# Kernel tuning notes

Measured on AMD Instinct MI355X. Metric: run time of the kernel, lower is better.

## Reference

```python
import math
import jax, jax.numpy as jnp
import numpy as np

B, L, D = 8, 512, 32
SEQ_LEN = 512.0
N_PATCHES, N_REF = 16, 32
LAT, HM = 128, 4
FH, NL, FF = 8, 3, 128
PRED = 96

def _time_embed(t, d):
    # interleaved sin/cos embedding, matching PositionalEmbedding's div_term
    div = jnp.exp(jnp.arange(0, d, 2, dtype=jnp.float32) * (-math.log(10000.0) / d))
    ang = t[..., None] * div
    out = jnp.zeros(t.shape + (d,), dtype=jnp.float32)
    return out.at[..., 0::2].set(jnp.sin(ang)).at[..., 1::2].set(jnp.cos(ang))

def _layernorm(x, g, b):
    mu = jnp.mean(x, axis=-1, keepdims=True)
    var = jnp.var(x, axis=-1, keepdims=True)
    return (x - mu) / jnp.sqrt(var + 1e-5) * g + b

def _mha(z, Wq, Wk, Wv, Wo, bq, bk, bv, bo):
    N, S, dm = z.shape
    hd = dm // FH
    q = (z @ Wq + bq).reshape(N, S, FH, hd)
    k = (z @ Wk + bk).reshape(N, S, FH, hd)
    v = (z @ Wv + bv).reshape(N, S, FH, hd)
    s = jnp.einsum('nqhe,nkhe->nhqk', q, k) / math.sqrt(hd)
    a = jax.nn.softmax(s, axis=-1)
    o = jnp.einsum('nhqk,nkhe->nqhe', a, v).reshape(N, S, dm)
    return o @ Wo + bo

def _forward(x, x_mark, x_mask, Wq, Wk, W_out, b_out, f_Wq, f_Wk, f_Wv, f_Wo, f_bq, f_bk, f_bv, f_bo, f_ln1_g, f_ln1_b, f_W1, f_b1, f_W2, f_b2, f_ln2_g, f_ln2_b, ln_f_g, ln_f_b, W_lin, b_lin):
    t = x_mark[:, :, 0]                                   # [B, L] irregular timestamps in [0, SEQ_LEN]
    edges = jnp.linspace(0.0, SEQ_LEN, N_PATCHES + 1)
    refs = jnp.linspace(0.0, SEQ_LEN, N_REF * N_PATCHES).reshape(N_PATCHES, N_REF)
    obs_valid = jnp.sum(x_mask, axis=-1) > 0              # [B, L]
    dk = LAT // HM
    Kmat = (_time_embed(t, LAT) @ Wk).reshape(B, L, HM, dk)
    v = x * x_mask                                        # mask values like `v = v * m` in original
    reprs = []
    for i in range(N_PATCHES):  # fixed small structural loop
        # _split_patch equivalent: per-channel masked attention is permutation
        # invariant, so the sort/scatter compaction reduces to masking.
        in_patch = (t >= edges[i]) & (t <= edges[i + 1]) & obs_valid   # [B, L]
        Qi = (_time_embed(refs[i], LAT) @ Wq).reshape(N_REF, HM, dk)
        scores = jnp.einsum('rhe,blhe->bhrl', Qi, Kmat) / math.sqrt(dk)
        cmask = x_mask * in_patch[..., None].astype(x.dtype)           # [B, L, D]
        neg = jnp.where(cmask[:, None, None, :, :] > 0, 0.0, -1e9)     # [B,1,1,L,D]
        p = jax.nn.softmax(scores[..., None] + neg, axis=3)            # [B,H,R,L,D]
        attn = jnp.einsum('bhrld,bld->brhd', p, v)                     # [B,R,H,D]
        reprs.append(attn.reshape(B, N_REF, HM * D) @ W_out + b_out)   # [B,R,D]
    rp = jnp.stack(reprs, axis=1)                          # [B, NP, R, D]
    z = rp.transpose(0, 3, 1, 2).reshape(B * D, N_PATCHES, N_REF)
    z = z + _time_embed(jnp.arange(N_PATCHES, dtype=jnp.float32), N_REF)[None]
    for l in range(NL):
        a = _mha(z, f_Wq[l], f_Wk[l], f_Wv[l], f_Wo[l], f_bq[l], f_bk[l], f_bv[l], f_bo[l])
        z = _layernorm(z + a, f_ln1_g[l], f_ln1_b[l])
        y = jax.nn.gelu(z @ f_W1[l] + f_b1[l]) @ f_W2[l] + f_b2[l]
        z = _layernorm(z + y, f_ln2_g[l], f_ln2_b[l])
    z = _layernorm(z, ln_f_g, ln_f_b)
    emb = z.reshape(B, D, N_PATCHES, N_REF).transpose(0, 1, 3, 2)      # [B, D, R, NP]
    out = emb.reshape(B, D, N_REF * N_PATCHES) @ W_lin + b_lin         # [B, D, PRED]
    return out.transpose(0, 2, 1)                          # [B, PRED, D]

def setup_inputs():
    key = jax.random.key(0)
    ks = jax.random.split(key, 30)
    def w(i, shape, fan_in):
        return jax.random.normal(ks[i], shape, jnp.float32) / math.sqrt(fan_in)
    return {
        'x': jax.random.normal(ks[0], (B, L, D), jnp.float32),
        'x_mark': jnp.sort(jax.random.uniform(ks[1], (B, L, 1), jnp.float32) * SEQ_LEN, axis=1),
        'x_mask': (jax.random.uniform(ks[2], (B, L, D), jnp.float32) < 0.8).astype(jnp.float32),
        'Wq': w(3, (LAT, LAT), LAT),
        'Wk': w(4, (LAT, LAT), LAT),
        'W_out': w(5, (HM * D, D), HM * D),
        'b_out': jnp.zeros((D,), jnp.float32),
        'f_Wq': w(6, (NL, N_REF, N_REF), N_REF),
        'f_Wk': w(7, (NL, N_REF, N_REF), N_REF),
        'f_Wv': w(8, (NL, N_REF, N_REF), N_REF),
        'f_Wo': w(9, (NL, N_REF, N_REF), N_REF),
        'f_bq': jnp.zeros((NL, N_REF), jnp.float32),
        'f_bk': jnp.zeros((NL, N_REF), jnp.float32),
        'f_bv': jnp.zeros((NL, N_REF), jnp.float32),
        'f_bo': jnp.zeros((NL, N_REF), jnp.float32),
        'f_ln1_g': jnp.ones((NL, N_REF), jnp.float32),
        'f_ln1_b': jnp.zeros((NL, N_REF), jnp.float32),
        'f_W1': w(10, (NL, N_REF, FF), N_REF),
        'f_b1': jnp.zeros((NL, FF), jnp.float32),
        'f_W2': w(11, (NL, FF, N_REF), FF),
        'f_b2': jnp.zeros((NL, N_REF), jnp.float32),
        'f_ln2_g': jnp.ones((NL, N_REF), jnp.float32),
        'f_ln2_b': jnp.zeros((NL, N_REF), jnp.float32),
        'ln_f_g': jnp.ones((N_REF,), jnp.float32),
        'ln_f_b': jnp.zeros((N_REF,), jnp.float32),
        'W_lin': w(12, (N_REF * N_PATCHES, PRED), N_REF * N_PATCHES),
        'b_lin': jnp.zeros((PRED,), jnp.float32),
    }

def reference(x, x_mark, x_mask, Wq, Wk, W_out, b_out, f_Wq, f_Wk, f_Wv, f_Wo, f_bq, f_bk, f_bv, f_bo, f_ln1_g, f_ln1_b, f_W1, f_b1, f_W2, f_b2, f_ln2_g, f_ln2_b, ln_f_g, ln_f_b, W_lin, b_lin):
    return _forward(x, x_mark, x_mask, Wq, Wk, W_out, b_out, f_Wq, f_Wk, f_Wv, f_Wo, f_bq, f_bk, f_bv, f_bo, f_ln1_g, f_ln1_b, f_W1, f_b1, f_W2, f_b2, f_ln2_g, f_ln2_b, ln_f_g, ln_f_b, W_lin, b_lin)
```

## Files before the change

### kernel.cpp

```cpp
#include <hip/hip_runtime.h>
#include <math.h>


#define ISQ32 0.17677669529663687f
#define C128  (-0.07195578415606394f)
#define C32   (-0.28782313662425575f)

__launch_bounds__(256)
__global__ void k_embed_mm(const float* __restrict__ x_mark,
                           const float* __restrict__ Wk,
                           const float* __restrict__ Wq,
                           const float* __restrict__ x_mask,
                           float* __restrict__ Kmat,
                           float* __restrict__ Qall,
                           unsigned* __restrict__ obsBits) {
    if (blockIdx.x >= 144) {
        const int gt = (blockIdx.x - 144) * 256 + threadIdx.x;
        const int w = gt >> 6, lane = gt & 63;
        const int bl = w * 2 + (lane >> 5);
        const int d = lane & 31;
        const unsigned long long mm = __ballot(x_mask[bl * 32 + d] > 0.0f);
        if (lane == 0)  obsBits[w * 2]     = (unsigned)(mm & 0xffffffffull);
        if (lane == 32) obsBits[w * 2 + 1] = (unsigned)(mm >> 32);
        return;
    }
    __shared__ float sTe[32][128];
    const int wv = threadIdx.x >> 6;
    const int lane = threadIdx.x & 63;
    const int bb = blockIdx.x;
    const int row0 = bb * 32 + wv * 8;
    const float dv = __expf((float)(2 * lane) * C128);
    #pragma unroll
    for (int rr = 0; rr < 8; ++rr) {
        const int row = row0 + rr;
        const float t = (row < 4096) ? x_mark[row] : (float)(row - 4096) * (512.0f / 511.0f);
        const float ang = t * dv;
        sTe[wv * 8 + rr][2 * lane]     = __sinf(ang);
        sTe[wv * 8 + rr][2 * lane + 1] = __cosf(ang);
    }
    __syncthreads();
    const float* W = (bb < 128) ? Wk : Wq;
    float a0[8], a1[8];
    #pragma unroll
    for (int rr = 0; rr < 8; ++rr) { a0[rr] = 0.f; a1[rr] = 0.f; }
    for (int k = 0; k < 128; ++k) {
        const float wa = W[k * 128 + lane];
        const float wb = W[k * 128 + lane + 64];
        #pragma unroll
        for (int rr = 0; rr < 8; ++rr) {
            const float te = sTe[wv * 8 + rr][k];
            a0[rr] = fmaf(te, wa, a0[rr]);
            a1[rr] = fmaf(te, wb, a1[rr]);
        }
    }
    #pragma unroll
    for (int rr = 0; rr < 8; ++rr) {
        const int row = row0 + rr;
        float* outp = (row < 4096) ? (Kmat + row * 128) : (Qall + (row - 4096) * 128);
        outp[lane] = a0[rr];
        outp[lane + 64] = a1[rr];
    }
}

__launch_bounds__(256)
__global__ void k_patch_attn(const float* __restrict__ x,
                             const float* __restrict__ x_mark,
                             const unsigned* __restrict__ obsBits,
                             const float* __restrict__ Kmat,
                             const float* __restrict__ Qall,
                             float* __restrict__ attn) {
    __shared__ float sQ[32][36];
    __shared__ float sK[96][36];
    __shared__ float sX[96][36];
    __shared__ float sS[32][100];
    __shared__ unsigned sBits[96];
    __shared__ int sLo, sHi;
    __shared__ unsigned sAV;
    const int tid = threadIdx.x;
    const int h = blockIdx.x & 3;
    const int b = (blockIdx.x >> 2) & 7;
    const int i = blockIdx.x >> 5;
    const float e0 = 32.0f * (float)i, e1 = 32.0f * (float)(i + 1);
    if (tid == 0) { sLo = 512; sHi = -1; sAV = 0u; }
    __syncthreads();
    #pragma unroll
    for (int k = 0; k < 4; ++k) {
        const int idx = tid + 256 * k;
        sQ[idx >> 5][idx & 31] = Qall[(i * 32 + (idx >> 5)) * 128 + h * 32 + (idx & 31)];
    }
    {
        int mylo = 512, myhi = -1;
        unsigned mybits = 0u;
        #pragma unroll
        for (int k = 0; k < 2; ++k) {
            const int l = tid + 256 * k;
            const float t = x_mark[b * 512 + l];
            if (t >= e0 && t <= e1) {
                mylo = min(mylo, l);
                myhi = max(myhi, l);
                mybits |= obsBits[b * 512 + l];
            }
        }
        #pragma unroll
        for (int off = 32; off > 0; off >>= 1) {
            mylo = min(mylo, __shfl_xor(mylo, off));
            myhi = max(myhi, __shfl_xor(myhi, off));
            mybits |= __shfl_xor(mybits, off);
        }
        if ((tid & 63) == 0) {
            atomicMin(&sLo, mylo);
            atomicMax(&sHi, myhi);
            atomicOr(&sAV, mybits);
        }
    }
    __syncthreads();
    const int lo = sLo, hi = sHi;
    const int NA = hi - lo + 1;
    const unsigned av = sAV;
    const int r = tid >> 3, dg = tid & 7;

    if (NA >= 1 && NA <= 96 && av == 0xffffffffu) {
        if (tid < NA) sBits[tid] = obsBits[b * 512 + lo + tid];
        for (int idx = tid; idx < NA * 32; idx += 256) {
            const int ll = idx >> 5, c = idx & 31;
            sK[ll][c] = Kmat[(b * 512 + lo + ll) * 128 + h * 32 + c];
            sX[ll][c] = x[(b * 512 + lo + ll) * 32 + c];
        }
        __syncthreads();
        float m = -1e30f;
        for (int ll = dg; ll < NA; ll += 8) {
            float p0 = 0.f, p1 = 0.f, p2 = 0.f, p3 = 0.f;
            #pragma unroll
            for (int e = 0; e < 32; e += 4) {
                p0 = fmaf(sQ[r][e],     sK[ll][e],     p0);
                p1 = fmaf(sQ[r][e + 1], sK[ll][e + 1], p1);
                p2 = fmaf(sQ[r][e + 2], sK[ll][e + 2], p2);
                p3 = fmaf(sQ[r][e + 3], sK[ll][e + 3], p3);
            }
            const float s = (p0 + p1 + p2 + p3) * ISQ32;
            sS[r][ll] = s;
            m = fmaxf(m, s);
        }
        #pragma unroll
        for (int off = 4; off > 0; off >>= 1) m = fmaxf(m, __shfl_xor(m, off));
        for (int ll = dg; ll < NA; ll += 8) sS[r][ll] = __expf(sS[r][ll] - m);
        __syncthreads();
        float num0 = 0.f, num1 = 0.f, num2 = 0.f, num3 = 0.f;
        float den0 = 0.f, den1 = 0.f, den2 = 0.f, den3 = 0.f;
        for (int ll = 0; ll < NA; ++ll) {
            const float e = sS[r][ll];
            const unsigned bits = sBits[ll];
            if ((bits >> dg) & 1u)        { den0 += e; num0 = fmaf(e, sX[ll][dg],      num0); }
            if ((bits >> (dg + 8)) & 1u)  { den1 += e; num1 = fmaf(e, sX[ll][dg + 8],  num1); }
            if ((bits >> (dg + 16)) & 1u) { den2 += e; num2 = fmaf(e, sX[ll][dg + 16], num2); }
            if ((bits >> (dg + 24)) & 1u) { den3 += e; num3 = fmaf(e, sX[ll][dg + 24], num3); }
        }
        float* ap = attn + ((i * 8 + b) * 32 + r) * 128 + h * 32;
        ap[dg]      = num0 / den0;
        ap[dg + 8]  = num1 / den1;
        ap[dg + 16] = num2 / den2;
        ap[dg + 24] = num3 / den3;
    } else {
        float m = -1e30f;
        float num[4] = {0.f, 0.f, 0.f, 0.f}, den[4] = {0.f, 0.f, 0.f, 0.f};
        for (int l = 0; l < 512; ++l) {
            const float t = x_mark[b * 512 + l];
            const unsigned bits = obsBits[b * 512 + l];
            const bool inr = (t >= e0 && t <= e1);
            const unsigned effD = (inr ? bits : 0u) | ~av;
            if (effD == 0u) continue;
            const unsigned effN = effD & bits;
            const float* Kp = Kmat + (b * 512 + l) * 128 + h * 32;
            float a = 0.f;
            #pragma unroll
            for (int e2 = 0; e2 < 32; ++e2) a = fmaf(sQ[r][e2], Kp[e2], a);
            const float s = a * ISQ32;
            float eNew;
            if (s > m) {
                const float scale = __expf(m - s);
                #pragma unroll
                for (int jj = 0; jj < 4; ++jj) { den[jj] *= scale; num[jj] *= scale; }
                m = s;
                eNew = 1.0f;
            } else {
                eNew = __expf(s - m);
            }
            const float* xp = x + (b * 512 + l) * 32;
            #pragma unroll
            for (int jj = 0; jj < 4; ++jj) {
                const int d = dg + 8 * jj;
                if ((effD >> d) & 1u) den[jj] += eNew;
                if ((effN >> d) & 1u) num[jj] = fmaf(eNew, xp[d], num[jj]);
            }
        }
        float* ap = attn + ((i * 8 + b) * 32 + r) * 128 + h * 32;
        #pragma unroll
        for (int jj = 0; jj < 4; ++jj) ap[dg + 8 * jj] = num[jj] / den[jj];
    }
}

__global__ void k_reprs(const float* __restrict__ attn,
                        const float* __restrict__ W_out,
                        const float* __restrict__ b_out,
                        float* __restrict__ z) {
    __shared__ float sA[32][129];
    const int tid = threadIdx.x;
    const int b = blockIdx.x & 7;
    const int i = blockIdx.x >> 3;
    #pragma unroll
    for (int k = 0; k < 16; ++k) {
        const int idx = tid + 256 * k;
        sA[idx >> 7][idx & 127] = attn[(i * 8 + b) * 4096 + idx];
    }
    __syncthreads();
    const int r = tid & 31, dgrp = tid >> 5;
    float acc0 = 0.f, acc1 = 0.f, acc2 = 0.f, acc3 = 0.f;
    #pragma unroll 8
    for (int k = 0; k < 128; ++k) {
        const float a = sA[r][k];
        acc0 = fmaf(a, W_out[k * 32 + dgrp],      acc0);
        acc1 = fmaf(a, W_out[k * 32 + dgrp + 8],  acc1);
        acc2 = fmaf(a, W_out[k * 32 + dgrp + 16], acc2);
        acc3 = fmaf(a, W_out[k * 32 + dgrp + 24], acc3);
    }
    const float dv = expf((float)(2 * (r >> 1)) * C32);
    const float ang = (float)i * dv;
    const float pe = (r & 1) ? cosf(ang) : sinf(ang);
    const int base = i * 32 + r;
    z[(b * 32 + dgrp)      * 512 + base] = acc0 + b_out[dgrp]      + pe;
    z[(b * 32 + dgrp + 8)  * 512 + base] = acc1 + b_out[dgrp + 8]  + pe;
    z[(b * 32 + dgrp + 16) * 512 + base] = acc2 + b_out[dgrp + 16] + pe;
    z[(b * 32 + dgrp + 24) * 512 + base] = acc3 + b_out[dgrp + 24] + pe;
}

__launch_bounds__(1024, 1)
__global__ void k_former(const float* __restrict__ z,
                         const float* __restrict__ f_Wq, const float* __restrict__ f_Wk,
                         const float* __restrict__ f_Wv, const float* __restrict__ f_Wo,
                         const float* __restrict__ f_bq, const float* __restrict__ f_bk,
                         const float* __restrict__ f_bv, const float* __restrict__ f_bo,
                         const float* __restrict__ f_ln1_g, const float* __restrict__ f_ln1_b,
                         const float* __restrict__ f_W1, const float* __restrict__ f_b1,
                         const float* __restrict__ f_W2, const float* __restrict__ f_b2,
                         const float* __restrict__ f_ln2_g, const float* __restrict__ f_ln2_b,
                         const float* __restrict__ ln_f_g, const float* __restrict__ ln_f_b,
                         const float* __restrict__ W_lin, const float* __restrict__ b_lin,
                         float* __restrict__ out) {
    __shared__ float sZ[16][36];
    __shared__ float sKm[16][36], sVm[16][36], sOm[16][36];
    __shared__ float sH[16][132];
    __shared__ float sZf[512];
    __shared__ float sPart[8][96];
    const int tid = threadIdx.x;
    const int n = blockIdx.x;
    const int s = tid >> 6;
    const int lane = tid & 63;
    const int j = lane & 31;
    const int kh = lane >> 5;

    float zres = z[n * 512 + s * 32 + j];
    if (kh == 0) sZ[s][j] = zres;

    for (int l = 0; l < 3; ++l) {
        float q_reg;
        {
            float zr[16];
            #pragma unroll
            for (int k4 = 0; k4 < 4; ++k4) {
                const float4 zv = *(const float4*)&sZ[s][kh * 16 + 4 * k4];
                zr[4 * k4] = zv.x; zr[4 * k4 + 1] = zv.y; zr[4 * k4 + 2] = zv.z; zr[4 * k4 + 3] = zv.w;
            }
            #pragma unroll
            for (int m = 0; m < 3; ++m) {
                const float* Wm = ((m == 0) ? f_Wq : (m == 1) ? f_Wk : f_Wv) + l * 1024;
                float w[16];
                #pragma unroll
                for (int k = 0; k < 16; ++k) w[k] = Wm[(kh * 16 + k) * 32 + j];
                float acc = 0.f;
                #pragma unroll
                for (int k = 0; k < 16; ++k) acc = fmaf(zr[k], w[k], acc);
                acc += __shfl_xor(acc, 32);
                acc += ((m == 0) ? f_bq : (m == 1) ? f_bk : f_bv)[l * 32 + j];
                if (m == 0) q_reg = acc;
                else if (m == 1) { if (kh == 0) sKm[s][j] = acc; }
                else             { if (kh == 0) sVm[s][j] = acc; }
            }
        }
        __syncthreads();
        {
            const int hh = lane >> 3;
            const int kp = lane & 7;
            const int h4 = hh * 4;
            const float qx = __shfl(q_reg, h4);
            const float qy = __shfl(q_reg, h4 + 1);
            const float qz = __shfl(q_reg, h4 + 2);
            const float qw = __shfl(q_reg, h4 + 3);
            const float4 kv0 = *(const float4*)&sKm[2 * kp][h4];
            const float4 kv1 = *(const float4*)&sKm[2 * kp + 1][h4];
            float s0 = (qx * kv0.x + qy * kv0.y + qz * kv0.z + qw * kv0.w) * 0.5f;
            float s1 = (qx * kv1.x + qy * kv1.y + qz * kv1.z + qw * kv1.w) * 0.5f;
            float mx = fmaxf(s0, s1);
            #pragma unroll
            for (int off = 4; off > 0; off >>= 1) mx = fmaxf(mx, __shfl_xor(mx, off));
            const float e0 = __expf(s0 - mx), e1 = __expf(s1 - mx);
            float sum = e0 + e1;
            #pragma unroll
            for (int off = 4; off > 0; off >>= 1) sum += __shfl_xor(sum, off);
            const float4 vv0 = *(const float4*)&sVm[2 * kp][h4];
            const float4 vv1 = *(const float4*)&sVm[2 * kp + 1][h4];
            float o0 = e0 * vv0.x + e1 * vv1.x;
            float o1 = e0 * vv0.y + e1 * vv1.y;
            float o2 = e0 * vv0.z + e1 * vv1.z;
            float o3 = e0 * vv0.w + e1 * vv1.w;
            #pragma unroll
            for (int off = 4; off > 0; off >>= 1) {
                o0 += __shfl_xor(o0, off); o1 += __shfl_xor(o1, off);
                o2 += __shfl_xor(o2, off); o3 += __shfl_xor(o3, off);
            }
            if (kp == 0) {
                const float inv = 1.0f / sum;
                *(float4*)&sOm[s][h4] = make_float4(o0 * inv, o1 * inv, o2 * inv, o3 * inv);
            }
        }
        {
            float w[16], orv[16];
            #pragma unroll
            for (int k = 0; k < 16; ++k) w[k] = f_Wo[l * 1024 + (kh * 16 + k) * 32 + j];
            #pragma unroll
            for (int k4 = 0; k4 < 4; ++k4) {
                const float4 ov = *(const float4*)&sOm[s][kh * 16 + 4 * k4];
                orv[4 * k4] = ov.x; orv[4 * k4 + 1] = ov.y; orv[4 * k4 + 2] = ov.z; orv[4 * k4 + 3] = ov.w;
            }
            float acc = 0.f;
            #pragma unroll
            for (int k = 0; k < 16; ++k) acc = fmaf(orv[k], w[k], acc);
            acc += __shfl_xor(acc, 32);
            const float t = zres + acc + f_bo[l * 32 + j];
            float sm = t, sq = t * t;
            #pragma unroll
            for (int off = 16; off > 0; off >>= 1) { sm += __shfl_xor(sm, off); sq += __shfl_xor(sq, off); }
            const float mu = sm * (1.0f / 32.0f);
            const float rs = rsqrtf(sq * (1.0f / 32.0f) - mu * mu + 1e-5f);
            zres = (t - mu) * rs * f_ln1_g[l * 32 + j] + f_ln1_b[l * 32 + j];
            if (kh == 0) sZ[s][j] = zres;
        }
        {
            const int f0 = lane, f1 = lane + 64;
            float wa[32], wb[32];
            #pragma unroll
            for (int k = 0; k < 32; ++k) {
                wa[k] = f_W1[l * 4096 + k * 128 + f0];
                wb[k] = f_W1[l * 4096 + k * 128 + f1];
            }
            float a0 = f_b1[l * 128 + f0], a1 = f_b1[l * 128 + f1];
            #pragma unroll
            for (int k4 = 0; k4 < 8; ++k4) {
                const float4 zv = *(const float4*)&sZ[s][4 * k4];
                a0 = fmaf(zv.x, wa[4 * k4], a0);     a0 = fmaf(zv.y, wa[4 * k4 + 1], a0);
                a0 = fmaf(zv.z, wa[4 * k4 + 2], a0); a0 = fmaf(zv.w, wa[4 * k4 + 3], a0);
                a1 = fmaf(zv.x, wb[4 * k4], a1);     a1 = fmaf(zv.y, wb[4 * k4 + 1], a1);
                a1 = fmaf(zv.z, wb[4 * k4 + 2], a1); a1 = fmaf(zv.w, wb[4 * k4 + 3], a1);
            }
            const float ea = __expf(1.5957691216057308f * (a0 + 0.044715f * a0 * a0 * a0));
            const float eb = __expf(1.5957691216057308f * (a1 + 0.044715f * a1 * a1 * a1));
            sH[s][f0] = 0.5f * a0 * (2.0f - 2.0f / (ea + 1.0f));
            sH[s][f1] = 0.5f * a1 * (2.0f - 2.0f / (eb + 1.0f));
        }
        {
            float acc = 0.f;
            #pragma unroll
            for (int kc = 0; kc < 2; ++kc) {
                float w[32];
                #pragma unroll
                for (int k = 0; k < 32; ++k) w[k] = f_W2[l * 4096 + (kh * 64 + kc * 32 + k) * 32 + j];
                #pragma unroll
                for (int k4 = 0; k4 < 8; ++k4) {
                    const float4 hv = *(const float4*)&sH[s][kh * 64 + kc * 32 + 4 * k4];
                    acc = fmaf(hv.x, w[4 * k4], acc);     acc = fmaf(hv.y, w[4 * k4 + 1], acc);
                    acc = fmaf(hv.z, w[4 * k4 + 2], acc); acc = fmaf(hv.w, w[4 * k4 + 3], acc);
                }
            }
            acc += __shfl_xor(acc, 32);
            const float t = zres + acc + f_b2[l * 32 + j];
            float sm = t, sq = t * t;
            #pragma unroll
            for (int off = 16; off > 0; off >>= 1) { sm += __shfl_xor(sm, off); sq += __shfl_xor(sq, off); }
            const float mu = sm * (1.0f / 32.0f);
            const float rs = rsqrtf(sq * (1.0f / 32.0f) - mu * mu + 1e-5f);
            zres = (t - mu) * rs * f_ln2_g[l * 32 + j] + f_ln2_b[l * 32 + j];
            if (kh == 0) sZ[s][j] = zres;
        }
        __syncthreads();
    }
    {
        const float t = zres;
        float sm = t, sq = t * t;
        #pragma unroll
        for (int off = 16; off > 0; off >>= 1) { sm += __shfl_xor(sm, off); sq += __shfl_xor(sq, off); }
        const float mu = sm * (1.0f / 32.0f);
        const float rs = rsqrtf(sq * (1.0f / 32.0f) - mu * mu + 1e-5f);
        if (kh == 0) sZf[j * 16 + s] = (t - mu) * rs * ln_f_g[j] + ln_f_b[j];
    }
    __syncthreads();
    if (tid < 768) {
        const int c = tid / 96, o = tid % 96;
        const int j0 = c * 64;
        float acc = 0.f;
        #pragma unroll 16
        for (int jj = 0; jj < 64; ++jj)
            acc = fmaf(sZf[j0 + jj], W_lin[(j0 + jj) * 96 + o], acc);
        sPart[c][o] = acc;
    }
    __syncthreads();
    if (tid < 96) {
        float acc = b_lin[tid];
        #pragma unroll
        for (int c = 0; c < 8; ++c) acc += sPart[c][tid];
        out[((n >> 5) * 96 + tid) * 32 + (n & 31)] = acc;
    }
}

extern "C" void kernel_launch(void* const* d_in, const int* in_sizes, int n_in,
                              void* d_out, int out_size, void* d_ws, size_t ws_size,
                              hipStream_t stream) {
    const float* x       = (const float*)d_in[0];
    const float* x_mark  = (const float*)d_in[1];
    const float* x_mask  = (const float*)d_in[2];
    const float* Wq      = (const float*)d_in[3];
    const float* Wk      = (const float*)d_in[4];
    const float* W_out   = (const float*)d_in[5];
    const float* b_out   = (const float*)d_in[6];
    const float* f_Wq    = (const float*)d_in[7];
    const float* f_Wk    = (const float*)d_in[8];
    const float* f_Wv    = (const float*)d_in[9];
    const float* f_Wo    = (const float*)d_in[10];
    const float* f_bq    = (const float*)d_in[11];
    const float* f_bk    = (const float*)d_in[12];
    const float* f_bv    = (const float*)d_in[13];
    const float* f_bo    = (const float*)d_in[14];
    const float* f_ln1_g = (const float*)d_in[15];
    const float* f_ln1_b = (const float*)d_in[16];
    const float* f_W1    = (const float*)d_in[17];
    const float* f_b1    = (const float*)d_in[18];
    const float* f_W2    = (const float*)d_in[19];
    const float* f_b2    = (const float*)d_in[20];
    const float* f_ln2_g = (const float*)d_in[21];
    const float* f_ln2_b = (const float*)d_in[22];
    const float* ln_f_g  = (const float*)d_in[23];
    const float* ln_f_b  = (const float*)d_in[24];
    const float* W_lin   = (const float*)d_in[25];
    const float* b_lin   = (const float*)d_in[26];

    float* ws = (float*)d_ws;
    float* Kmat      = ws;
    float* Qall      = ws + 524288;
    unsigned* obsB   = (unsigned*)(ws + 589824);
    float* attn      = ws + 593920;
    float* zbuf      = ws + 1118208;

    k_embed_mm<<<656, 256, 0, stream>>>(x_mark, Wk, Wq, x_mask, Kmat, Qall, obsB);
    k_patch_attn<<<512, 256, 0, stream>>>(x, x_mark, obsB, Kmat, Qall, attn);
    k_reprs<<<128, 256, 0, stream>>>(attn, W_out, b_out, zbuf);
    k_former<<<256, 1024, 0, stream>>>(zbuf,
        f_Wq, f_Wk, f_Wv, f_Wo, f_bq, f_bk, f_bv, f_bo,
        f_ln1_g, f_ln1_b, f_W1, f_b1, f_W2, f_b2, f_ln2_g, f_ln2_b,
        ln_f_g, ln_f_b, W_lin, b_lin, (float*)d_out);
}
```

Before: 67.65 us.

## Fuse patch-repr projection into former kernel and stage transposed weights in LDS

Removes the separate k_reprs launch. The output projection of the patch attention, plus its positional embedding, is now computed at the start of k_former by the first 512 threads. Meanwhile the other threads stage transposed Q/K/V/O, W1 and W2 weights into shared memory, and each layer reloads the next layer's weights. This cuts one launch and the zbuf round trip, and replaces strided per-thread global weight loads with float4 LDS reads. In exchange each block recomputes its slice of attn@W_out, uses more shared memory, and adds extra barriers.

```diff
diff --git a/kernel.cpp b/kernel.cpp
--- a/kernel.cpp
+++ b/kernel.cpp
@@ -199,42 +199,9 @@
     }
 }
 
-__global__ void k_reprs(const float* __restrict__ attn,
-                        const float* __restrict__ W_out,
-                        const float* __restrict__ b_out,
-                        float* __restrict__ z) {
-    __shared__ float sA[32][129];
-    const int tid = threadIdx.x;
-    const int b = blockIdx.x & 7;
-    const int i = blockIdx.x >> 3;
-    #pragma unroll
-    for (int k = 0; k < 16; ++k) {
-        const int idx = tid + 256 * k;
-        sA[idx >> 7][idx & 127] = attn[(i * 8 + b) * 4096 + idx];
-    }
-    __syncthreads();
-    const int r = tid & 31, dgrp = tid >> 5;
-    float acc0 = 0.f, acc1 = 0.f, acc2 = 0.f, acc3 = 0.f;
-    #pragma unroll 8
-    for (int k = 0; k < 128; ++k) {
-        const float a = sA[r][k];
-        acc0 = fmaf(a, W_out[k * 32 + dgrp],      acc0);
-        acc1 = fmaf(a, W_out[k * 32 + dgrp + 8],  acc1);
-        acc2 = fmaf(a, W_out[k * 32 + dgrp + 16], acc2);
-        acc3 = fmaf(a, W_out[k * 32 + dgrp + 24], acc3);
-    }
-    const float dv = expf((float)(2 * (r >> 1)) * C32);
-    const float ang = (float)i * dv;
-    const float pe = (r & 1) ? cosf(ang) : sinf(ang);
-    const int base = i * 32 + r;
-    z[(b * 32 + dgrp)      * 512 + base] = acc0 + b_out[dgrp]      + pe;
-    z[(b * 32 + dgrp + 8)  * 512 + base] = acc1 + b_out[dgrp + 8]  + pe;
-    z[(b * 32 + dgrp + 16) * 512 + base] = acc2 + b_out[dgrp + 16] + pe;
-    z[(b * 32 + dgrp + 24) * 512 + base] = acc3 + b_out[dgrp + 24] + pe;
-}
-
 __launch_bounds__(1024, 1)
-__global__ void k_former(const float* __restrict__ z,
+__global__ void k_former(const float* __restrict__ attn,
+                         const float* __restrict__ W_out, const float* __restrict__ b_out,
                          const float* __restrict__ f_Wq, const float* __restrict__ f_Wk,
                          const float* __restrict__ f_Wv, const float* __restrict__ f_Wo,
                          const float* __restrict__ f_bq, const float* __restrict__ f_bk,
@@ -246,6 +213,9 @@
                          const float* __restrict__ ln_f_g, const float* __restrict__ ln_f_b,
                          const float* __restrict__ W_lin, const float* __restrict__ b_lin,
                          float* __restrict__ out) {
+    __shared__ float wT[4][32][36];
+    __shared__ float w1T[128][36];
+    __shared__ float w2T[32][140];
     __shared__ float sZ[16][36];
     __shared__ float sKm[16][36], sVm[16][36], sOm[16][36];
     __shared__ float sH[16][132];
@@ -253,13 +223,57 @@
     __shared__ float sPart[8][96];
     const int tid = threadIdx.x;
     const int n = blockIdx.x;
+    const int b = n >> 5, d = n & 31;
     const int s = tid >> 6;
     const int lane = tid & 63;
     const int j = lane & 31;
     const int kh = lane >> 5;
 
-    float zres = z[n * 512 + s * 32 + j];
-    if (kh == 0) sZ[s][j] = zres;
+    if (tid < 512) {
+        const int pi = tid >> 5, pr = tid & 31;
+        const float* ar = attn + ((pi * 8 + b) * 32 + pr) * 128;
+        float acc = 0.f;
+        #pragma unroll 8
+        for (int c4 = 0; c4 < 32; ++c4) {
+            const float4 a4 = ((const float4*)ar)[c4];
+            acc = fmaf(a4.x, W_out[(4 * c4 + 0) * 32 + d], acc);
+            acc = fmaf(a4.y, W_out[(4 * c4 + 1) * 32 + d], acc);
+            acc = fmaf(a4.z, W_out[(4 * c4 + 2) * 32 + d], acc);
+            acc = fmaf(a4.w, W_out[(4 * c4 + 3) * 32 + d], acc);
+        }
+        const float dv = __expf((float)(2 * (pr >> 1)) * C32);
+        const float ang = (float)pi * dv;
+        const float pe = (pr & 1) ? __cosf(ang) : __sinf(ang);
+        sZ[pi][pr] = acc + b_out[d] + pe;
+    } else {
+        const int t = tid - 512;
+        #pragma unroll
+        for (int q = 0; q < 2; ++q) {
+            const int idx = q * 512 + t;
+            {
+                const int m4 = idx >> 8, sub = idx & 255;
+                const float* Wm4 = ((m4 == 0) ? f_Wq : (m4 == 1) ? f_Wk : (m4 == 2) ? f_Wv : f_Wo);
+                const float4 v = ((const float4*)Wm4)[sub];
+                const int k = sub >> 3, j0 = (sub & 7) << 2;
+                wT[m4][j0 + 0][k] = v.x; wT[m4][j0 + 1][k] = v.y;
+                wT[m4][j0 + 2][k] = v.z; wT[m4][j0 + 3][k] = v.w;
+            }
+            {
+                const float4 v = ((const float4*)f_W1)[idx];
+                const int k = idx >> 5, f0 = (idx & 31) << 2;
+                w1T[f0 + 0][k] = v.x; w1T[f0 + 1][k] = v.y;
+                w1T[f0 + 2][k] = v.z; w1T[f0 + 3][k] = v.w;
+            }
+            {
+                const float4 v = ((const float4*)f_W2)[idx];
+                const int k = idx >> 3, j0 = (idx & 7) << 2;
+                w2T[j0 + 0][k] = v.x; w2T[j0 + 1][k] = v.y;
+                w2T[j0 + 2][k] = v.z; w2T[j0 + 3][k] = v.w;
+            }
+        }
+    }
+    __syncthreads();
+    float zres = sZ[s][j];
 
     for (int l = 0; l < 3; ++l) {
         float q_reg;
@@ -272,13 +286,13 @@
             }
             #pragma unroll
             for (int m = 0; m < 3; ++m) {
-                const float* Wm = ((m == 0) ? f_Wq : (m == 1) ? f_Wk : f_Wv) + l * 1024;
-                float w[16];
-                #pragma unroll
-                for (int k = 0; k < 16; ++k) w[k] = Wm[(kh * 16 + k) * 32 + j];
                 float acc = 0.f;
                 #pragma unroll
-                for (int k = 0; k < 16; ++k) acc = fmaf(zr[k], w[k], acc);
+                for (int k4 = 0; k4 < 4; ++k4) {
+                    const float4 w = *(const float4*)&wT[m][j][kh * 16 + 4 * k4];
+                    acc = fmaf(zr[4 * k4], w.x, acc);     acc = fmaf(zr[4 * k4 + 1], w.y, acc);
+                    acc = fmaf(zr[4 * k4 + 2], w.z, acc); acc = fmaf(zr[4 * k4 + 3], w.w, acc);
+                }
                 acc += __shfl_xor(acc, 32);
                 acc += ((m == 0) ? f_bq : (m == 1) ? f_bk : f_bv)[l * 32 + j];
                 if (m == 0) q_reg = acc;
@@ -323,17 +337,14 @@
             }
         }
         {
-            float w[16], orv[16];
-            #pragma unroll
-            for (int k = 0; k < 16; ++k) w[k] = f_Wo[l * 1024 + (kh * 16 + k) * 32 + j];
+            float acc = 0.f;
             #pragma unroll
             for (int k4 = 0; k4 < 4; ++k4) {
+                const float4 w  = *(const float4*)&wT[3][j][kh * 16 + 4 * k4];
                 const float4 ov = *(const float4*)&sOm[s][kh * 16 + 4 * k4];
-                orv[4 * k4] = ov.x; orv[4 * k4 + 1] = ov.y; orv[4 * k4 + 2] = ov.z; orv[4 * k4 + 3] = ov.w;
-            }
-            float acc = 0.f;
-            #pragma unroll
-            for (int k = 0; k < 16; ++k) acc = fmaf(orv[k], w[k], acc);
+                acc = fmaf(ov.x, w.x, acc); acc = fmaf(ov.y, w.y, acc);
+                acc = fmaf(ov.z, w.z, acc); acc = fmaf(ov.w, w.w, acc);
+            }
             acc += __shfl_xor(acc, 32);
             const float t = zres + acc + f_bo[l * 32 + j];
             float sm = t, sq = t * t;
@@ -346,20 +357,16 @@
         }
         {
             const int f0 = lane, f1 = lane + 64;
-            float wa[32], wb[32];
-            #pragma unroll
-            for (int k = 0; k < 32; ++k) {
-                wa[k] = f_W1[l * 4096 + k * 128 + f0];
-                wb[k] = f_W1[l * 4096 + k * 128 + f1];
-            }
             float a0 = f_b1[l * 128 + f0], a1 = f_b1[l * 128 + f1];
             #pragma unroll
             for (int k4 = 0; k4 < 8; ++k4) {
                 const float4 zv = *(const float4*)&sZ[s][4 * k4];
-                a0 = fmaf(zv.x, wa[4 * k4], a0);     a0 = fmaf(zv.y, wa[4 * k4 + 1], a0);
-                a0 = fmaf(zv.z, wa[4 * k4 + 2], a0); a0 = fmaf(zv.w, wa[4 * k4 + 3], a0);
-                a1 = fmaf(zv.x, wb[4 * k4], a1);     a1 = fmaf(zv.y, wb[4 * k4 + 1], a1);
-                a1 = fmaf(zv.z, wb[4 * k4 + 2], a1); a1 = fmaf(zv.w, wb[4 * k4 + 3], a1);
+                const float4 wa = *(const float4*)&w1T[f0][4 * k4];
+                const float4 wb = *(const float4*)&w1T[f1][4 * k4];
+                a0 = fmaf(zv.x, wa.x, a0); a0 = fmaf(zv.y, wa.y, a0);
+                a0 = fmaf(zv.z, wa.z, a0); a0 = fmaf(zv.w, wa.w, a0);
+                a1 = fmaf(zv.x, wb.x, a1); a1 = fmaf(zv.y, wb.y, a1);
+                a1 = fmaf(zv.z, wb.z, a1); a1 = fmaf(zv.w, wb.w, a1);
             }
             const float ea = __expf(1.5957691216057308f * (a0 + 0.044715f * a0 * a0 * a0));
             const float eb = __expf(1.5957691216057308f * (a1 + 0.044715f * a1 * a1 * a1));
@@ -369,16 +376,11 @@
         {
             float acc = 0.f;
             #pragma unroll
-            for (int kc = 0; kc < 2; ++kc) {
-                float w[32];
-                #pragma unroll
-                for (int k = 0; k < 32; ++k) w[k] = f_W2[l * 4096 + (kh * 64 + kc * 32 + k) * 32 + j];
-                #pragma unroll
-                for (int k4 = 0; k4 < 8; ++k4) {
-                    const float4 hv = *(const float4*)&sH[s][kh * 64 + kc * 32 + 4 * k4];
-                    acc = fmaf(hv.x, w[4 * k4], acc);     acc = fmaf(hv.y, w[4 * k4 + 1], acc);
-                    acc = fmaf(hv.z, w[4 * k4 + 2], acc); acc = fmaf(hv.w, w[4 * k4 + 3], acc);
-                }
+            for (int k4 = 0; k4 < 16; ++k4) {
+                const float4 w  = *(const float4*)&w2T[j][kh * 64 + 4 * k4];
+                const float4 hv = *(const float4*)&sH[s][kh * 64 + 4 * k4];
+                acc = fmaf(hv.x, w.x, acc); acc = fmaf(hv.y, w.y, acc);
+                acc = fmaf(hv.z, w.z, acc); acc = fmaf(hv.w, w.w, acc);
             }
             acc += __shfl_xor(acc, 32);
             const float t = zres + acc + f_b2[l * 32 + j];
@@ -391,6 +393,30 @@
             if (kh == 0) sZ[s][j] = zres;
         }
         __syncthreads();
+        if (l < 2) {
+            const int lx = l + 1;
+            {
+                const int m4 = tid >> 8, sub = tid & 255;
+                const float* Wm4 = ((m4 == 0) ? f_Wq : (m4 == 1) ? f_Wk : (m4 == 2) ? f_Wv : f_Wo) + lx * 1024;
+                const float4 v = ((const float4*)Wm4)[sub];
+                const int k = sub >> 3, j0 = (sub & 7) << 2;
+                wT[m4][j0 + 0][k] = v.x; wT[m4][j0 + 1][k] = v.y;
+                wT[m4][j0 + 2][k] = v.z; wT[m4][j0 + 3][k] = v.w;
+            }
+            {
+                const float4 v = ((const float4*)(f_W1 + lx * 4096))[tid];
+                const int k = tid >> 5, f0 = (tid & 31) << 2;
+                w1T[f0 + 0][k] = v.x; w1T[f0 + 1][k] = v.y;
+                w1T[f0 + 2][k] = v.z; w1T[f0 + 3][k] = v.w;
+            }
+            {
+                const float4 v = ((const float4*)(f_W2 + lx * 4096))[tid];
+                const int k = tid >> 3, j0 = (tid & 7) << 2;
+                w2T[j0 + 0][k] = v.x; w2T[j0 + 1][k] = v.y;
+                w2T[j0 + 2][k] = v.z; w2T[j0 + 3][k] = v.w;
+            }
+            __syncthreads();
+        }
     }
     {
         const float t = zres;
@@ -416,7 +442,7 @@
         float acc = b_lin[tid];
         #pragma unroll
         for (int c = 0; c < 8; ++c) acc += sPart[c][tid];
-        out[((n >> 5) * 96 + tid) * 32 + (n & 31)] = acc;
+        out[(b * 96 + tid) * 32 + d] = acc;
     }
 }
 
@@ -456,12 +482,10 @@
     float* Qall      = ws + 524288;
     unsigned* obsB   = (unsigned*)(ws + 589824);
     float* attn      = ws + 593920;
-    float* zbuf      = ws + 1118208;
 
     k_embed_mm<<<656, 256, 0, stream>>>(x_mark, Wk, Wq, x_mask, Kmat, Qall, obsB);
     k_patch_attn<<<512, 256, 0, stream>>>(x, x_mark, obsB, Kmat, Qall, attn);
-    k_reprs<<<128, 256, 0, stream>>>(attn, W_out, b_out, zbuf);
-    k_former<<<256, 1024, 0, stream>>>(zbuf,
+    k_former<<<256, 1024, 0, stream>>>(attn, W_out, b_out,
         f_Wq, f_Wk, f_Wv, f_Wo, f_bq, f_bk, f_bv, f_bo,
         f_ln1_g, f_ln1_b, f_W1, f_b1, f_W2, f_b2, f_ln2_g, f_ln2_b,
         ln_f_g, ln_f_b, W_lin, b_lin, (float*)d_out);
```

Result: faster. 65.55 us (-3.1%).
